# Kernel tuning notes

Hardware: AMD Instinct MI355X
Metric: run time of the kernel (lower is better)

The kernel has to match this reference:

```python
import jax, jax.numpy as jnp
import numpy as np

N = 50000        # nodes
E = 800000       # edges (before self loops)
F_IN = 64        # num_features
DIM = 64         # num_hidden
C = 10           # num_classes
G = 256          # graphs in batch
NEG_SLOPE = 0.2


def setup_inputs() -> dict:
    key = jax.random.key(0)
    ks = jax.random.split(key, 20)
    def w(k, shape, fan_in):
        return jax.random.normal(k, shape, dtype=jnp.float32) / np.sqrt(fan_in)
    x = jax.random.normal(ks[0], (N, F_IN), dtype=jnp.float32)
    edge_index = jax.random.randint(ks[1], (2, E), 0, N, dtype=jnp.int64)
    batch = jnp.sort(jax.random.randint(ks[2], (N,), 0, G, dtype=jnp.int64))
    return {
        "x": x, "edge_index": edge_index, "batch": batch,
        "w1": w(ks[3], (F_IN, DIM), F_IN), "as1": w(ks[4], (DIM,), DIM), "ad1": w(ks[5], (DIM,), DIM), "b1": jnp.zeros((DIM,), jnp.float32),
        "w2": w(ks[6], (DIM, DIM), DIM),  "as2": w(ks[7], (DIM,), DIM), "ad2": w(ks[8], (DIM,), DIM), "b2": jnp.zeros((DIM,), jnp.float32),
        "w3": w(ks[9], (DIM, DIM), DIM),  "as3": w(ks[10], (DIM,), DIM), "ad3": w(ks[11], (DIM,), DIM), "b3": jnp.zeros((DIM,), jnp.float32),
        "fc1_w": w(ks[12], (DIM, DIM), DIM), "fc1_b": jnp.zeros((DIM,), jnp.float32),
        "fc2_w": w(ks[13], (DIM, C), DIM),   "fc2_b": jnp.zeros((C,), jnp.float32),
    }


def _gat_conv(x, src, dst, w, a_src, a_dst, b, n_nodes):
    # PyG GATConv, heads=1: h = x W; e_ij = LeakyReLU(a_src.h_j + a_dst.h_i);
    # alpha = segment-softmax over edges grouped by target i; out_i = sum_j alpha_ij h_j + b
    h = x @ w                                   # [N, DIM]
    alpha_s = h @ a_src                         # [N]
    alpha_d = h @ a_dst                         # [N]
    e = jax.nn.leaky_relu(alpha_s[src] + alpha_d[dst], NEG_SLOPE)  # [E']
    e_max = jax.ops.segment_max(e, dst, num_segments=n_nodes)
    e_exp = jnp.exp(e - e_max[dst])
    denom = jax.ops.segment_sum(e_exp, dst, num_segments=n_nodes)
    alpha = e_exp / (denom[dst] + 1e-16)        # [E']
    out = jax.ops.segment_sum(alpha[:, None] * h[src], dst, num_segments=n_nodes)
    return out + b


def _l2_normalize(x):
    nrm = jnp.linalg.norm(x, axis=1, keepdims=True)
    return x / jnp.maximum(nrm, 1e-12)


def reference(x, edge_index, batch, w1, as1, ad1, b1, w2, as2, ad2, b2,
              w3, as3, ad3, b3, fc1_w, fc1_b, fc2_w, fc2_b):
    n = x.shape[0]
    loops = jnp.arange(n, dtype=edge_index.dtype)
    src = jnp.concatenate([edge_index[0], loops])   # add_self_loops=True (PyG default)
    dst = jnp.concatenate([edge_index[1], loops])
    h = _gat_conv(x, src, dst, w1, as1, ad1, b1, n)
    h = jax.nn.relu(_l2_normalize(h))
    h = _gat_conv(h, src, dst, w2, as2, ad2, b2, n)
    h = jax.nn.relu(_l2_normalize(h))
    h = _gat_conv(h, src, dst, w3, as3, ad3, b3, n)
    h = jax.nn.relu(_l2_normalize(h))
    g = jax.ops.segment_sum(h, batch, num_segments=G)   # global_add_pool -> [G, DIM]
    g = jax.nn.relu(g @ fc1_w + fc1_b)
    logits = g @ fc2_w + fc2_b
    return jax.nn.log_softmax(logits, axis=-1)
```

## Files before the change

### kernel.cpp

```cpp
#include <hip/hip_runtime.h>
#include <hip/hip_bf16.h>
#include <math.h>

#define DIM 64
#define GNUM 256
#define CNUM 10

__device__ __forceinline__ unsigned bfpack(float a, float b) {
    unsigned ua = __builtin_bit_cast(unsigned, a);
    unsigned ub = __builtin_bit_cast(unsigned, b);
    ua += 0x7fffu + ((ua >> 16) & 1u);
    ub += 0x7fffu + ((ub >> 16) & 1u);
    return (ua >> 16) | (ub & 0xffff0000u);
}
__device__ __forceinline__ float bflo(unsigned u) { return __builtin_bit_cast(float, u << 16); }
__device__ __forceinline__ float bfhi(unsigned u) { return __builtin_bit_cast(float, u & 0xffff0000u); }
__device__ __forceinline__ float bfs(unsigned short u) { return __builtin_bit_cast(float, (unsigned)u << 16); }

__global__ void deg_rank_kernel(const int* __restrict__ ei, int E, int N,
                                int* __restrict__ deg, int* __restrict__ rank) {
    int i = blockIdx.x * blockDim.x + threadIdx.x;
    int EP = E + N;
    if (i >= EP) return;
    int d = (i < E) ? ei[E + i] : (i - E);
    rank[i] = atomicAdd(&deg[d], 1);
}

__global__ __launch_bounds__(256) void scan_misc(const int* __restrict__ deg, int* __restrict__ part, int n, int nb,
                                                 const int* __restrict__ batch, int N,
                                                 int* __restrict__ gstart) {
    int bid = blockIdx.x;
    if (bid < nb) {
        __shared__ int ws[4];
        int i = bid * 256 + threadIdx.x;
        int v = (i < n) ? deg[i] : 0;
        #pragma unroll
        for (int d = 32; d >= 1; d >>= 1) v += __shfl_xor(v, d);
        if ((threadIdx.x & 63) == 0) ws[threadIdx.x >> 6] = v;
        __syncthreads();
        if (threadIdx.x == 0) part[bid] = ws[0] + ws[1] + ws[2] + ws[3];
    } else {
        for (int g = threadIdx.x; g <= GNUM; g += 256) {
            int lo = 0, hi = N;
            while (lo < hi) { int mid = (lo + hi) >> 1; if (batch[mid] < g) lo = mid + 1; else hi = mid; }
            gstart[g] = lo;
        }
    }
}

__global__ __launch_bounds__(256) void scan_down(const int* __restrict__ deg, const int* __restrict__ part,
                                                 int* __restrict__ offs, int n) {
    __shared__ int ws[4];
    __shared__ int base_s;
    int tid = threadIdx.x, lane = tid & 63, wid = tid >> 6;
    int pv = (tid < (int)blockIdx.x) ? part[tid] : 0;
    #pragma unroll
    for (int d = 32; d >= 1; d >>= 1) pv += __shfl_xor(pv, d);
    if (lane == 0) ws[wid] = pv;
    __syncthreads();
    if (tid == 0) base_s = ws[0] + ws[1] + ws[2] + ws[3];
    __syncthreads();
    int i = blockIdx.x * 256 + tid;
    int v = (i < n) ? deg[i] : 0;
    int x = v;
    #pragma unroll
    for (int d = 1; d < 64; d <<= 1) { int t = __shfl_up(x, d); if (lane >= d) x += t; }
    if (lane == 63) ws[wid] = x;
    __syncthreads();
    int add = base_s;
    for (int w = 0; w < wid; ++w) add += ws[w];
    if (i < n) offs[i] = add + x - v;
    if (i == n - 1) offs[n] = add + x;
}

#define XSTR 68
template<bool BF16IN>
__device__ __forceinline__ void mm_tile_body(int bid,
                                             const void* __restrict__ in_, const float* __restrict__ W,
                                             const float* __restrict__ a_s, const float* __restrict__ a_d,
                                             unsigned* __restrict__ hb, float* __restrict__ as_,
                                             float* __restrict__ ad_, int N) {
    __shared__ float Ws[DIM * DIM];
    __shared__ float xT[XSTR * DIM];
    int tid = threadIdx.x;
    int base = bid * 64;

    const float4* W4 = (const float4*)W;
    float4* Ws4 = (float4*)Ws;
    #pragma unroll
    for (int i = 0; i < 4; ++i) Ws4[tid + 256 * i] = W4[tid + 256 * i];

    {
        int row = tid >> 2;
        int kb = (tid & 3) << 4;
        int grow = base + row;
        int crow = grow < N ? grow : N - 1;
        if (BF16IN) {
            const unsigned* xr = (const unsigned*)in_ + ((size_t)crow << 5) + (kb >> 1);
            uint4 u0 = *(const uint4*)xr;
            uint4 u1 = *(const uint4*)(xr + 4);
            xT[(kb + 0) * XSTR + row] = bflo(u0.x);  xT[(kb + 1) * XSTR + row] = bfhi(u0.x);
            xT[(kb + 2) * XSTR + row] = bflo(u0.y);  xT[(kb + 3) * XSTR + row] = bfhi(u0.y);
            xT[(kb + 4) * XSTR + row] = bflo(u0.z);  xT[(kb + 5) * XSTR + row] = bfhi(u0.z);
            xT[(kb + 6) * XSTR + row] = bflo(u0.w);  xT[(kb + 7) * XSTR + row] = bfhi(u0.w);
            xT[(kb + 8) * XSTR + row] = bflo(u1.x);  xT[(kb + 9) * XSTR + row] = bfhi(u1.x);
            xT[(kb + 10) * XSTR + row] = bflo(u1.y); xT[(kb + 11) * XSTR + row] = bfhi(u1.y);
            xT[(kb + 12) * XSTR + row] = bflo(u1.z); xT[(kb + 13) * XSTR + row] = bfhi(u1.z);
            xT[(kb + 14) * XSTR + row] = bflo(u1.w); xT[(kb + 15) * XSTR + row] = bfhi(u1.w);
        } else {
            const float4* xr = (const float4*)((const float*)in_ + ((size_t)crow << 6) + kb);
            float4 v0 = xr[0], v1 = xr[1], v2 = xr[2], v3 = xr[3];
            xT[(kb + 0) * XSTR + row] = v0.x;  xT[(kb + 1) * XSTR + row] = v0.y;
            xT[(kb + 2) * XSTR + row] = v0.z;  xT[(kb + 3) * XSTR + row] = v0.w;
            xT[(kb + 4) * XSTR + row] = v1.x;  xT[(kb + 5) * XSTR + row] = v1.y;
            xT[(kb + 6) * XSTR + row] = v1.z;  xT[(kb + 7) * XSTR + row] = v1.w;
            xT[(kb + 8) * XSTR + row] = v2.x;  xT[(kb + 9) * XSTR + row] = v2.y;
            xT[(kb + 10) * XSTR + row] = v2.z; xT[(kb + 11) * XSTR + row] = v2.w;
            xT[(kb + 12) * XSTR + row] = v3.x; xT[(kb + 13) * XSTR + row] = v3.y;
            xT[(kb + 14) * XSTR + row] = v3.z; xT[(kb + 15) * XSTR + row] = v3.w;
        }
    }
    __syncthreads();

    int tx = tid & 15, ty = tid >> 4;
    int c0 = tx << 2, r0 = ty << 2;
    float acc[4][4] = {{0.f}};
    #pragma unroll 8
    for (int k = 0; k < DIM; ++k) {
        float4 xv = *(const float4*)(xT + k * XSTR + r0);
        float4 wv = *(const float4*)(Ws + k * DIM + c0);
        acc[0][0] += xv.x * wv.x; acc[0][1] += xv.x * wv.y; acc[0][2] += xv.x * wv.z; acc[0][3] += xv.x * wv.w;
        acc[1][0] += xv.y * wv.x; acc[1][1] += xv.y * wv.y; acc[1][2] += xv.y * wv.z; acc[1][3] += xv.y * wv.w;
        acc[2][0] += xv.z * wv.x; acc[2][1] += xv.z * wv.y; acc[2][2] += xv.z * wv.z; acc[2][3] += xv.z * wv.w;
        acc[3][0] += xv.w * wv.x; acc[3][1] += xv.w * wv.y; acc[3][2] += xv.w * wv.z; acc[3][3] += xv.w * wv.w;
    }

    float4 av = *(const float4*)(a_s + c0);
    float4 dv = *(const float4*)(a_d + c0);
    #pragma unroll
    for (int ri = 0; ri < 4; ++ri) {
        int grow = base + r0 + ri;
        float s1 = acc[ri][0] * av.x + acc[ri][1] * av.y + acc[ri][2] * av.z + acc[ri][3] * av.w;
        float s2 = acc[ri][0] * dv.x + acc[ri][1] * dv.y + acc[ri][2] * dv.z + acc[ri][3] * dv.w;
        #pragma unroll
        for (int d = 1; d <= 8; d <<= 1) { s1 += __shfl_xor(s1, d); s2 += __shfl_xor(s2, d); }
        if (grow < N) {
            uint2 o;
            o.x = bfpack(acc[ri][0], acc[ri][1]);
            o.y = bfpack(acc[ri][2], acc[ri][3]);
            *(uint2*)(hb + ((size_t)grow << 5) + (tx << 1)) = o;
            if (tx == 0) { as_[grow] = s1; ad_[grow] = s2; }
        }
    }
}

__global__ __launch_bounds__(256) void mm_tile_bf(const unsigned* __restrict__ in, const float* __restrict__ W,
                                                  const float* __restrict__ a_s, const float* __restrict__ a_d,
                                                  unsigned* __restrict__ hb, float* __restrict__ as_,
                                                  float* __restrict__ ad_, int N) {
    mm_tile_body<true>(blockIdx.x, in, W, a_s, a_d, hb, as_, ad_, N);
}

__global__ __launch_bounds__(256) void mm_fill(const float* __restrict__ in, const float* __restrict__ W,
                                               const float* __restrict__ a_s, const float* __restrict__ a_d,
                                               unsigned* __restrict__ hb, float* __restrict__ as_,
                                               float* __restrict__ ad_, int N, int nbt,
                                               const int* __restrict__ ei, const int* __restrict__ rank, int E,
                                               const int* __restrict__ offs, int* __restrict__ csr_src) {
    int bid = blockIdx.x;
    if (bid < nbt) {
        mm_tile_body<false>(bid, in, W, a_s, a_d, hb, as_, ad_, N);
    } else {
        int i = (bid - nbt) * 256 + threadIdx.x;
        int EP = E + N;
        if (i >= EP) return;
        int s, d;
        if (i < E) { s = ei[i]; d = ei[E + i]; } else { s = i - E; d = i - E; }
        csr_src[offs[d] + rank[i]] = s;
    }
}

__global__ __launch_bounds__(256) void gat_agg(const unsigned* __restrict__ hb, const float* __restrict__ as_,
                                               const float* __restrict__ ad_, const int* __restrict__ offs,
                                               const int* __restrict__ csr, const float* __restrict__ bias,
                                               unsigned* __restrict__ outb, int N) {
    int tid = threadIdx.x, lane = tid & 63, wid = tid >> 6;
    int node = blockIdx.x * 4 + wid;
    if (node >= N) return;
    int start = offs[node], end = offs[node + 1];
    int deg = end - start;
    float adi = ad_[node];

    int src_reg = 0;
    float w_reg = 0.f;
    if (lane < deg) {
        src_reg = csr[start + lane];
        float e = as_[src_reg] + adi;
        e = (e > 0.f) ? e : 0.2f * e;
        w_reg = expf(e);
    }

    int esub = lane >> 4, fg = lane & 15;
    int dmain = deg < 64 ? deg : 64;
    float a0 = 0.f, a1 = 0.f, a2 = 0.f, a3 = 0.f, sw = 0.f;
    for (int i0 = 0; i0 < dmain; i0 += 16) {
        float wA = __shfl(w_reg, i0 + esub);
        int   sA = __shfl(src_reg, i0 + esub);
        float wB = __shfl(w_reg, i0 + 4 + esub);
        int   sB = __shfl(src_reg, i0 + 4 + esub);
        float wC = __shfl(w_reg, i0 + 8 + esub);
        int   sC = __shfl(src_reg, i0 + 8 + esub);
        float wD = __shfl(w_reg, i0 + 12 + esub);
        int   sD = __shfl(src_reg, i0 + 12 + esub);
        const uint2 hA = *(const uint2*)(hb + ((size_t)sA << 5) + (fg << 1));
        const uint2 hB = *(const uint2*)(hb + ((size_t)sB << 5) + (fg << 1));
        const uint2 hC = *(const uint2*)(hb + ((size_t)sC << 5) + (fg << 1));
        const uint2 hD = *(const uint2*)(hb + ((size_t)sD << 5) + (fg << 1));
        sw += wA + wB + wC + wD;
        a0 += wA * bflo(hA.x) + wB * bflo(hB.x) + wC * bflo(hC.x) + wD * bflo(hD.x);
        a1 += wA * bfhi(hA.x) + wB * bfhi(hB.x) + wC * bfhi(hC.x) + wD * bfhi(hD.x);
        a2 += wA * bflo(hA.y) + wB * bflo(hB.y) + wC * bflo(hC.y) + wD * bflo(hD.y);
        a3 += wA * bfhi(hA.y) + wB * bfhi(hB.y) + wC * bfhi(hC.y) + wD * bfhi(hD.y);
    }
    for (int t0 = start + 64; t0 < end; t0 += 4) {
        int t = t0 + esub;
        float w = 0.f; int src = 0;
        if (t < end) {
            src = csr[t];
            float e = as_[src] + adi;
            e = (e > 0.f) ? e : 0.2f * e;
            w = expf(e);
        }
        const uint2 hv = *(const uint2*)(hb + ((size_t)src << 5) + (fg << 1));
        sw += w;
        a0 += w * bflo(hv.x); a1 += w * bfhi(hv.x);
        a2 += w * bflo(hv.y); a3 += w * bfhi(hv.y);
    }
    #pragma unroll
    for (int d = 16; d <= 32; d <<= 1) {
        a0 += __shfl_xor(a0, d); a1 += __shfl_xor(a1, d);
        a2 += __shfl_xor(a2, d); a3 += __shfl_xor(a3, d);
        sw += __shfl_xor(sw, d);
    }
    float inv = 1.f / (sw + 1e-16f);
    const float4 bv = *(const float4*)(bias + (fg << 2));
    float o0 = a0 * inv + bv.x, o1 = a1 * inv + bv.y, o2 = a2 * inv + bv.z, o3 = a3 * inv + bv.w;
    float n2 = o0 * o0 + o1 * o1 + o2 * o2 + o3 * o3;
    #pragma unroll
    for (int d = 1; d <= 8; d <<= 1) n2 += __shfl_xor(n2, d);
    float innrm = 1.f / fmaxf(sqrtf(n2), 1e-12f);
    if (esub == 0) {
        uint2 o;
        o.x = bfpack(fmaxf(o0 * innrm, 0.f), fmaxf(o1 * innrm, 0.f));
        o.y = bfpack(fmaxf(o2 * innrm, 0.f), fmaxf(o3 * innrm, 0.f));
        *(uint2*)(outb + ((size_t)node << 5) + (fg << 1)) = o;
    }
}

__global__ __launch_bounds__(256) void pool_mlp(const unsigned short* __restrict__ hb, const int* __restrict__ gstart,
                                                const float* __restrict__ fc1w, const float* __restrict__ fc1b,
                                                const float* __restrict__ fc2w, const float* __restrict__ fc2b,
                                                float* __restrict__ out) {
    __shared__ float W1[DIM * DIM];
    __shared__ float red[4 * DIM];
    __shared__ float tbuf[DIM];
    __shared__ float obuf[CNUM];
    int tid = threadIdx.x, lane = tid & 63, wv = tid >> 6;
    int gid = blockIdx.x;

    const float4* W4 = (const float4*)fc1w;
    float4* W1s = (float4*)W1;
    #pragma unroll
    for (int i = 0; i < 4; ++i) W1s[tid + 256 * i] = W4[tid + 256 * i];

    int s = gstart[gid], e = gstart[gid + 1];
    float acc = 0.f;
    for (int i = s + wv; i < e; i += 4) acc += bfs(hb[((size_t)i << 6) + lane]);
    red[wv * DIM + lane] = acc;
    __syncthreads();

    if (wv == 0) {
        float g = red[lane] + red[DIM + lane] + red[2 * DIM + lane] + red[3 * DIM + lane];
        float t = fc1b[lane];
        #pragma unroll
        for (int k = 0; k < DIM; ++k) t += __shfl(g, k) * W1[k * DIM + lane];
        t = fmaxf(t, 0.f);
        tbuf[lane] = t;
        float o = 0.f;
        if (lane < CNUM) {
            o = fc2b[lane];
            #pragma unroll
            for (int k = 0; k < DIM; ++k) o += tbuf[k] * fc2w[k * CNUM + lane];
            obuf[lane] = o;
        }
        if (lane < CNUM) {
            float mx = obuf[0];
            #pragma unroll
            for (int k = 1; k < CNUM; ++k) mx = fmaxf(mx, obuf[k]);
            float ssum = 0.f;
            #pragma unroll
            for (int k = 0; k < CNUM; ++k) ssum += expf(obuf[k] - mx);
            out[gid * CNUM + lane] = o - mx - logf(ssum);
        }
    }
}

static inline size_t align256(size_t x) { return (x + 255) & ~size_t(255); }

extern "C" void kernel_launch(void* const* d_in, const int* in_sizes, int n_in,
                              void* d_out, int out_size, void* d_ws, size_t ws_size,
                              hipStream_t stream) {
    const float* x     = (const float*)d_in[0];
    const int*   ei    = (const int*)d_in[1];
    const int*   batch = (const int*)d_in[2];
    const float* w1  = (const float*)d_in[3];
    const float* as1 = (const float*)d_in[4];
    const float* ad1 = (const float*)d_in[5];
    const float* b1  = (const float*)d_in[6];
    const float* w2  = (const float*)d_in[7];
    const float* as2 = (const float*)d_in[8];
    const float* ad2 = (const float*)d_in[9];
    const float* b2  = (const float*)d_in[10];
    const float* w3  = (const float*)d_in[11];
    const float* as3 = (const float*)d_in[12];
    const float* ad3 = (const float*)d_in[13];
    const float* b3  = (const float*)d_in[14];
    const float* fc1w = (const float*)d_in[15];
    const float* fc1b = (const float*)d_in[16];
    const float* fc2w = (const float*)d_in[17];
    const float* fc2b = (const float*)d_in[18];
    float* out = (float*)d_out;

    int N  = in_sizes[0] / DIM;
    int E  = in_sizes[1] / 2;
    int EP = E + N;
    int nb = (N + 255) / 256;

    char* p = (char*)d_ws;
    unsigned* hbf = (unsigned*)p; p += align256(sizeof(unsigned) * (size_t)N * (DIM / 2));
    unsigned* oAb = (unsigned*)p; p += align256(sizeof(unsigned) * (size_t)N * (DIM / 2));
    unsigned* oBb = (unsigned*)p; p += align256(sizeof(unsigned) * (size_t)N * (DIM / 2));
    float* as_  = (float*)p; p += align256(sizeof(float) * (size_t)N);
    float* ad_  = (float*)p; p += align256(sizeof(float) * (size_t)N);
    int*   deg  = (int*)p;   p += align256(sizeof(int) * (size_t)N);
    int*   offs = (int*)p;   p += align256(sizeof(int) * (size_t)(N + 1));
    int*   rank = (int*)p;   p += align256(sizeof(int) * (size_t)EP);
    int*   csr  = (int*)p;   p += align256(sizeof(int) * (size_t)EP);
    int*   part = (int*)p;   p += align256(sizeof(int) * (size_t)nb);
    int*   gst  = (int*)p;   p += align256(sizeof(int) * (size_t)(GNUM + 1));

    int nblk = (N + 3) / 4;
    int nbt = (N + 63) / 64;
    int epBlocks = (EP + 255) / 256;

    hipMemsetAsync(deg, 0, sizeof(int) * (size_t)N, stream);
    deg_rank_kernel<<<epBlocks, 256, 0, stream>>>(ei, E, N, deg, rank);
    scan_misc<<<nb + 1, 256, 0, stream>>>(deg, part, N, nb, batch, N, gst);
    scan_down<<<nb, 256, 0, stream>>>(deg, part, offs, N);

    mm_fill<<<nbt + epBlocks, 256, 0, stream>>>(x, w1, as1, ad1, hbf, as_, ad_, N, nbt,
                                                ei, rank, E, offs, csr);
    gat_agg<<<nblk, 256, 0, stream>>>(hbf, as_, ad_, offs, csr, b1, oAb, N);
    mm_tile_bf<<<nbt, 256, 0, stream>>>(oAb, w2, as2, ad2, hbf, as_, ad_, N);
    gat_agg<<<nblk, 256, 0, stream>>>(hbf, as_, ad_, offs, csr, b2, oBb, N);
    mm_tile_bf<<<nbt, 256, 0, stream>>>(oBb, w3, as3, ad3, hbf, as_, ad_, N);
    gat_agg<<<nblk, 256, 0, stream>>>(hbf, as_, ad_, offs, csr, b3, oAb, N);

    pool_mlp<<<GNUM, 256, 0, stream>>>((const unsigned short*)oAb, gst, fc1w, fc1b, fc2w, fc2b, out);
}
```

Baseline: 288.0 us.

## Precompute edge attention weights in separate pass and pack two nodes per wave

Edge attention weights (LeakyReLU and exp of as[src]+ad[dst]) now come from a new per-edge kernel that writes packed (src, weight) pairs. To support this, the CSR stores (src,dst) int2 pairs. The aggregation kernel now handles two nodes per 64-lane wave, with 16-lane groups each reading four consecutive edges. This removes the shuffle-based weight broadcast and the serialized tail loop for high-degree nodes, and doubles lane utilisation for the typical degree of about 17. In exchange there are three extra kernel launches and extra global traffic for the edge array, and the edge array is padded so over-reads stay in bounds.

```diff
diff --git a/kernel.cpp b/kernel.cpp
--- a/kernel.cpp
+++ b/kernel.cpp
@@ -166,7 +166,7 @@
                                                unsigned* __restrict__ hb, float* __restrict__ as_,
                                                float* __restrict__ ad_, int N, int nbt,
                                                const int* __restrict__ ei, const int* __restrict__ rank, int E,
-                                               const int* __restrict__ offs, int* __restrict__ csr_src) {
+                                               const int* __restrict__ offs, int2* __restrict__ csr_sd) {
     int bid = blockIdx.x;
     if (bid < nbt) {
         mm_tile_body<false>(bid, in, W, a_s, a_d, hb, as_, ad_, N);
@@ -176,72 +176,61 @@
         if (i >= EP) return;
         int s, d;
         if (i < E) { s = ei[i]; d = ei[E + i]; } else { s = i - E; d = i - E; }
-        csr_src[offs[d] + rank[i]] = s;
-    }
-}
-
-__global__ __launch_bounds__(256) void gat_agg(const unsigned* __restrict__ hb, const float* __restrict__ as_,
-                                               const float* __restrict__ ad_, const int* __restrict__ offs,
-                                               const int* __restrict__ csr, const float* __restrict__ bias,
+        csr_sd[offs[d] + rank[i]] = make_int2(s, d);
+    }
+}
+
+__global__ __launch_bounds__(256) void edge_w(const int2* __restrict__ csr_sd,
+                                              const float* __restrict__ as_,
+                                              const float* __restrict__ ad_,
+                                              int2* __restrict__ ews, int EP) {
+    int i = blockIdx.x * 256 + threadIdx.x;
+    if (i < 16) ews[EP + i] = make_int2(0, 0);
+    if (i >= EP) return;
+    int2 sd = csr_sd[i];
+    float e = as_[sd.x] + ad_[sd.y];
+    e = (e > 0.f) ? e : 0.2f * e;
+    float w = expf(e);
+    ews[i] = make_int2(sd.x, __builtin_bit_cast(int, w));
+}
+
+__global__ __launch_bounds__(256) void gat_agg(const unsigned* __restrict__ hb,
+                                               const int2* __restrict__ ews,
+                                               const int* __restrict__ offs,
+                                               const float* __restrict__ bias,
                                                unsigned* __restrict__ outb, int N) {
     int tid = threadIdx.x, lane = tid & 63, wid = tid >> 6;
-    int node = blockIdx.x * 4 + wid;
-    if (node >= N) return;
-    int start = offs[node], end = offs[node + 1];
-    int deg = end - start;
-    float adi = ad_[node];
-
-    int src_reg = 0;
-    float w_reg = 0.f;
-    if (lane < deg) {
-        src_reg = csr[start + lane];
-        float e = as_[src_reg] + adi;
-        e = (e > 0.f) ? e : 0.2f * e;
-        w_reg = expf(e);
-    }
-
-    int esub = lane >> 4, fg = lane & 15;
-    int dmain = deg < 64 ? deg : 64;
+    int half = lane >> 5;
+    int node = blockIdx.x * 8 + wid * 2 + half;
+    int esub = (lane >> 4) & 1, fg = lane & 15;
+    int start = 0, deg = 0;
+    if (node < N) { start = offs[node]; deg = offs[node + 1] - start; }
+
     float a0 = 0.f, a1 = 0.f, a2 = 0.f, a3 = 0.f, sw = 0.f;
-    for (int i0 = 0; i0 < dmain; i0 += 16) {
-        float wA = __shfl(w_reg, i0 + esub);
-        int   sA = __shfl(src_reg, i0 + esub);
-        float wB = __shfl(w_reg, i0 + 4 + esub);
-        int   sB = __shfl(src_reg, i0 + 4 + esub);
-        float wC = __shfl(w_reg, i0 + 8 + esub);
-        int   sC = __shfl(src_reg, i0 + 8 + esub);
-        float wD = __shfl(w_reg, i0 + 12 + esub);
-        int   sD = __shfl(src_reg, i0 + 12 + esub);
-        const uint2 hA = *(const uint2*)(hb + ((size_t)sA << 5) + (fg << 1));
-        const uint2 hB = *(const uint2*)(hb + ((size_t)sB << 5) + (fg << 1));
-        const uint2 hC = *(const uint2*)(hb + ((size_t)sC << 5) + (fg << 1));
-        const uint2 hD = *(const uint2*)(hb + ((size_t)sD << 5) + (fg << 1));
+    for (int i0 = 0; i0 < deg; i0 += 8) {
+        int eb = i0 + (esub << 2);
+        int t = start + eb;
+        int2 eA = ews[t];
+        int2 eB = ews[t + 1];
+        int2 eC = ews[t + 2];
+        int2 eD = ews[t + 3];
+        float wA = (eb + 0 < deg) ? __builtin_bit_cast(float, eA.y) : 0.f;
+        float wB = (eb + 1 < deg) ? __builtin_bit_cast(float, eB.y) : 0.f;
+        float wC = (eb + 2 < deg) ? __builtin_bit_cast(float, eC.y) : 0.f;
+        float wD = (eb + 3 < deg) ? __builtin_bit_cast(float, eD.y) : 0.f;
+        const uint2 hA = *(const uint2*)(hb + ((size_t)eA.x << 5) + (fg << 1));
+        const uint2 hB = *(const uint2*)(hb + ((size_t)eB.x << 5) + (fg << 1));
+        const uint2 hC = *(const uint2*)(hb + ((size_t)eC.x << 5) + (fg << 1));
+        const uint2 hD = *(const uint2*)(hb + ((size_t)eD.x << 5) + (fg << 1));
         sw += wA + wB + wC + wD;
         a0 += wA * bflo(hA.x) + wB * bflo(hB.x) + wC * bflo(hC.x) + wD * bflo(hD.x);
         a1 += wA * bfhi(hA.x) + wB * bfhi(hB.x) + wC * bfhi(hC.x) + wD * bfhi(hD.x);
         a2 += wA * bflo(hA.y) + wB * bflo(hB.y) + wC * bflo(hC.y) + wD * bflo(hD.y);
         a3 += wA * bfhi(hA.y) + wB * bfhi(hB.y) + wC * bfhi(hC.y) + wD * bfhi(hD.y);
     }
-    for (int t0 = start + 64; t0 < end; t0 += 4) {
-        int t = t0 + esub;
-        float w = 0.f; int src = 0;
-        if (t < end) {
-            src = csr[t];
-            float e = as_[src] + adi;
-            e = (e > 0.f) ? e : 0.2f * e;
-            w = expf(e);
-        }
-        const uint2 hv = *(const uint2*)(hb + ((size_t)src << 5) + (fg << 1));
-        sw += w;
-        a0 += w * bflo(hv.x); a1 += w * bfhi(hv.x);
-        a2 += w * bflo(hv.y); a3 += w * bfhi(hv.y);
-    }
-    #pragma unroll
-    for (int d = 16; d <= 32; d <<= 1) {
-        a0 += __shfl_xor(a0, d); a1 += __shfl_xor(a1, d);
-        a2 += __shfl_xor(a2, d); a3 += __shfl_xor(a3, d);
-        sw += __shfl_xor(sw, d);
-    }
+    a0 += __shfl_xor(a0, 16); a1 += __shfl_xor(a1, 16);
+    a2 += __shfl_xor(a2, 16); a3 += __shfl_xor(a3, 16);
+    sw += __shfl_xor(sw, 16);
     float inv = 1.f / (sw + 1e-16f);
     const float4 bv = *(const float4*)(bias + (fg << 2));
     float o0 = a0 * inv + bv.x, o1 = a1 * inv + bv.y, o2 = a2 * inv + bv.z, o3 = a3 * inv + bv.w;
@@ -249,7 +238,7 @@
     #pragma unroll
     for (int d = 1; d <= 8; d <<= 1) n2 += __shfl_xor(n2, d);
     float innrm = 1.f / fmaxf(sqrtf(n2), 1e-12f);
-    if (esub == 0) {
+    if (esub == 0 && node < N) {
         uint2 o;
         o.x = bfpack(fmaxf(o0 * innrm, 0.f), fmaxf(o1 * innrm, 0.f));
         o.y = bfpack(fmaxf(o2 * innrm, 0.f), fmaxf(o3 * innrm, 0.f));
@@ -345,11 +334,12 @@
     int*   deg  = (int*)p;   p += align256(sizeof(int) * (size_t)N);
     int*   offs = (int*)p;   p += align256(sizeof(int) * (size_t)(N + 1));
     int*   rank = (int*)p;   p += align256(sizeof(int) * (size_t)EP);
-    int*   csr  = (int*)p;   p += align256(sizeof(int) * (size_t)EP);
+    int2*  csr_sd = (int2*)p; p += align256(sizeof(int2) * (size_t)EP);
+    int2*  ews  = (int2*)p;  p += align256(sizeof(int2) * (size_t)(EP + 16));
     int*   part = (int*)p;   p += align256(sizeof(int) * (size_t)nb);
     int*   gst  = (int*)p;   p += align256(sizeof(int) * (size_t)(GNUM + 1));
 
-    int nblk = (N + 3) / 4;
+    int nblk = (N + 7) / 8;
     int nbt = (N + 63) / 64;
     int epBlocks = (EP + 255) / 256;
 
@@ -359,12 +349,15 @@
     scan_down<<<nb, 256, 0, stream>>>(deg, part, offs, N);
 
     mm_fill<<<nbt + epBlocks, 256, 0, stream>>>(x, w1, as1, ad1, hbf, as_, ad_, N, nbt,
-                                                ei, rank, E, offs, csr);
-    gat_agg<<<nblk, 256, 0, stream>>>(hbf, as_, ad_, offs, csr, b1, oAb, N);
+                                                ei, rank, E, offs, csr_sd);
+    edge_w<<<epBlocks, 256, 0, stream>>>(csr_sd, as_, ad_, ews, EP);
+    gat_agg<<<nblk, 256, 0, stream>>>(hbf, ews, offs, b1, oAb, N);
     mm_tile_bf<<<nbt, 256, 0, stream>>>(oAb, w2, as2, ad2, hbf, as_, ad_, N);
-    gat_agg<<<nblk, 256, 0, stream>>>(hbf, as_, ad_, offs, csr, b2, oBb, N);
+    edge_w<<<epBlocks, 256, 0, stream>>>(csr_sd, as_, ad_, ews, EP);
+    gat_agg<<<nblk, 256, 0, stream>>>(hbf, ews, offs, b2, oBb, N);
     mm_tile_bf<<<nbt, 256, 0, stream>>>(oBb, w3, as3, ad3, hbf, as_, ad_, N);
-    gat_agg<<<nblk, 256, 0, stream>>>(hbf, as_, ad_, offs, csr, b3, oAb, N);
+    edge_w<<<epBlocks, 256, 0, stream>>>(csr_sd, as_, ad_, ews, EP);
+    gat_agg<<<nblk, 256, 0, stream>>>(hbf, ews, offs, b3, oAb, N);
 
     pool_mlp<<<GNUM, 256, 0, stream>>>((const unsigned short*)oAb, gst, fc1w, fc1b, fc2w, fc2b, out);
 }
```

Result: no change. 290.5 us (+0.9%).
